# Kernel optimization log

Measured on AMD Instinct MI355X. Metric: run time of the kernel, lower is better.

The kernel has to match this reference:

```python
import jax, jax.numpy as jnp
import numpy as np

N_NODES = 50000
N_REL = 3
N_EDGES = 400000


def _graph_conv(x, src, dst, W, b, n_nodes):
    """DGL GraphConv with norm='both': D_out^-1/2 gather-sum D_in^-1/2 (x W) + b."""
    ones = jnp.ones(src.shape[0], dtype=x.dtype)
    deg_out = jnp.clip(jax.ops.segment_sum(ones, src, num_segments=n_nodes), 1.0)
    deg_in = jnp.clip(jax.ops.segment_sum(ones, dst, num_segments=n_nodes), 1.0)
    h = x * jax.lax.rsqrt(deg_out)[:, None]          # [N, F_in] src-side norm
    h = h @ W                                        # [N, F_out] project before aggregate
    m = jax.ops.segment_sum(h[src], dst, num_segments=n_nodes)  # SpMM message passing
    return m * jax.lax.rsqrt(deg_in)[:, None] + b


def setup_inputs() -> dict:
    key = jax.random.key(0)
    k = jax.random.split(key, 6)
    x = jax.random.normal(k[0], (N_NODES, 128), dtype=jnp.float32)
    edges = jax.random.randint(k[1], (N_REL, 2, N_EDGES), 0, N_NODES, dtype=jnp.int32)
    W1 = jax.random.normal(k[2], (N_REL, 128, 128), dtype=jnp.float32) * (1.0 / np.sqrt(128))
    b1 = jnp.zeros((N_REL, 128), dtype=jnp.float32)
    W2 = jax.random.normal(k[3], (N_REL, 128, 64), dtype=jnp.float32) * (1.0 / np.sqrt(128))
    b2 = jnp.zeros((N_REL, 64), dtype=jnp.float32)
    return {"x": x, "edges": edges, "W1": W1, "b1": b1, "W2": W2, "b2": b2}


def reference(x, edges, W1, b1, W2, b2):
    n = x.shape[0]
    # Layer 1: HeteroGraphConv(sum over relations) then ReLU
    h = jnp.zeros((n, W1.shape[-1]), dtype=x.dtype)
    for r in range(N_REL):
        h = h + _graph_conv(x, edges[r, 0], edges[r, 1], W1[r], b1[r], n)
    h = jax.nn.relu(h)
    # Layer 2 (conv6): HeteroGraphConv(sum over relations)
    out = jnp.zeros((n, W2.shape[-1]), dtype=x.dtype)
    for r in range(N_REL):
        out = out + _graph_conv(h, edges[r, 0], edges[r, 1], W2[r], b2[r], n)
    return out
```

## Files before the change

### kernel.cpp

```cpp
#include <hip/hip_runtime.h>

constexpr int NN = 50000;
constexpr int NREL = 3;
constexpr int NE = 400000;
constexpr int CAP = 24;
constexpr int MAXSPILL = 4096;

constexpr int G1X = (NN + 63) / 64;
constexpr int GEMM1_BLKS = G1X * 2 * NREL;
constexpr int LDA = 68;

__device__ __forceinline__ float b2f(unsigned short u) {
  union { unsigned int i; float f; } v; v.i = (unsigned int)u << 16; return v.f;
}
__device__ __forceinline__ unsigned short f2b(float f) {
  union { float f; unsigned int i; } v; v.f = f;
  unsigned int r = v.i + 0x7fffu + ((v.i >> 16) & 1u);
  return (unsigned short)(r >> 16);
}

template <bool SCALE, bool INBF>
__device__ __forceinline__ void gemm_body(
    const void* __restrict__ Av, const float* __restrict__ W,
    const int* __restrict__ cnt_scale, unsigned short* __restrict__ C,
    int M, int N, int row0, int col0) {
  __shared__ float As[64][LDA];
  __shared__ float Bs[64][64];
  int t = threadIdx.x;
  int tx4 = (t & 15) << 2;
  int ty4 = (t >> 4) << 2;
  float acc[4][4] = {};
  for (int k0 = 0; k0 < 128; k0 += 64) {
    if (k0) __syncthreads();
#pragma unroll
    for (int i = 0; i < 4; ++i) {
      int idx = t + i * 256;
      int r = idx >> 4;
      int c4 = (idx & 15) << 2;
      int grow = row0 + r;
      float4 v = make_float4(0.f, 0.f, 0.f, 0.f);
      if (grow < M) {
        if (INBF) {
          ushort4 u = *(const ushort4*)((const unsigned short*)Av + (size_t)grow * 128 + k0 + c4);
          v = make_float4(b2f(u.x), b2f(u.y), b2f(u.z), b2f(u.w));
        } else {
          v = *(const float4*)((const float*)Av + (size_t)grow * 128 + k0 + c4);
        }
        if (SCALE) {
          float s = rsqrtf((float)max(cnt_scale[grow], 1));
          v.x *= s; v.y *= s; v.z *= s; v.w *= s;
        }
      }
      *(float4*)(&As[r][c4]) = v;
    }
#pragma unroll
    for (int i = 0; i < 4; ++i) {
      int idx = t + i * 256;
      int k = idx >> 4;
      int c4 = (idx & 15) << 2;
      *(float4*)(&Bs[k][c4]) = *(const float4*)(W + (size_t)(k0 + k) * N + col0 + c4);
    }
    __syncthreads();
#pragma unroll 8
    for (int k = 0; k < 64; k += 4) {
      float4 b0 = *(const float4*)(&Bs[k + 0][tx4]);
      float4 b1 = *(const float4*)(&Bs[k + 1][tx4]);
      float4 b2 = *(const float4*)(&Bs[k + 2][tx4]);
      float4 b3 = *(const float4*)(&Bs[k + 3][tx4]);
#pragma unroll
      for (int m = 0; m < 4; ++m) {
        float4 a = *(const float4*)(&As[ty4 + m][k]);
        acc[m][0] += a.x * b0.x + a.y * b1.x + a.z * b2.x + a.w * b3.x;
        acc[m][1] += a.x * b0.y + a.y * b1.y + a.z * b2.y + a.w * b3.y;
        acc[m][2] += a.x * b0.z + a.y * b1.z + a.z * b2.z + a.w * b3.z;
        acc[m][3] += a.x * b0.w + a.y * b1.w + a.z * b2.w + a.w * b3.w;
      }
    }
  }
#pragma unroll
  for (int m = 0; m < 4; ++m) {
    int row = row0 + ty4 + m;
    if (row < M) {
      ushort4 o;
      o.x = f2b(acc[m][0]); o.y = f2b(acc[m][1]);
      o.z = f2b(acc[m][2]); o.w = f2b(acc[m][3]);
      *(ushort4*)(C + (size_t)row * N + col0 + tx4) = o;
    }
  }
}

__global__ __launch_bounds__(256, 3) void fused_build_gemm1_kernel(
    const int* __restrict__ edges, int* __restrict__ cnt_out, int* __restrict__ cnt_in,
    unsigned short* __restrict__ ell, int* __restrict__ nspill, int* __restrict__ spill,
    const float* __restrict__ x, const float* __restrict__ W1, unsigned short* __restrict__ proj1) {
  __shared__ float As[64][LDA];
  __shared__ float Bs[64][64];
  int t = threadIdx.x;

  int eg = blockIdx.x * 256 + t;
  bool have = (eg < NREL * NE);
  int er = 0, es = 0, ed = 0;
  if (have) {
    er = eg / NE;
    int e = eg - er * NE;
    const int* b = edges + (size_t)er * 2 * NE;
    es = b[e];
    ed = b[NE + e];
  }

  int g = blockIdx.x;
  int r = g / (G1X * 2);
  int rem = g - r * (G1X * 2);
  int row0 = (rem >> 1) * 64;
  int col0 = (rem & 1) * 64;
  const float* W = W1 + (size_t)r * 128 * 128;
  unsigned short* C = proj1 + (size_t)r * NN * 128;

  int tx4 = (t & 15) << 2;
  int ty4 = (t >> 4) << 2;
  float acc[4][4] = {};
  int pos = 0;
  for (int k0 = 0; k0 < 128; k0 += 64) {
    if (k0) __syncthreads();
#pragma unroll
    for (int i = 0; i < 4; ++i) {
      int idx = t + i * 256;
      int rr = idx >> 4;
      int c4 = (idx & 15) << 2;
      int grow = row0 + rr;
      float4 v = make_float4(0.f, 0.f, 0.f, 0.f);
      if (grow < NN) v = *(const float4*)(x + (size_t)grow * 128 + k0 + c4);
      *(float4*)(&As[rr][c4]) = v;
    }
#pragma unroll
    for (int i = 0; i < 4; ++i) {
      int idx = t + i * 256;
      int k = idx >> 4;
      int c4 = (idx & 15) << 2;
      *(float4*)(&Bs[k][c4]) = *(const float4*)(W + (size_t)(k0 + k) * 128 + col0 + c4);
    }
    __syncthreads();
    if (k0 == 0 && have) {
      atomicAdd(cnt_out + er * NN + es, 1);
      pos = atomicAdd(cnt_in + er * NN + ed, 1);
    }
#pragma unroll 8
    for (int k = 0; k < 64; k += 4) {
      float4 b0 = *(const float4*)(&Bs[k + 0][tx4]);
      float4 b1 = *(const float4*)(&Bs[k + 1][tx4]);
      float4 b2 = *(const float4*)(&Bs[k + 2][tx4]);
      float4 b3 = *(const float4*)(&Bs[k + 3][tx4]);
#pragma unroll
      for (int m = 0; m < 4; ++m) {
        float4 a = *(const float4*)(&As[ty4 + m][k]);
        acc[m][0] += a.x * b0.x + a.y * b1.x + a.z * b2.x + a.w * b3.x;
        acc[m][1] += a.x * b0.y + a.y * b1.y + a.z * b2.y + a.w * b3.y;
        acc[m][2] += a.x * b0.z + a.y * b1.z + a.z * b2.z + a.w * b3.z;
        acc[m][3] += a.x * b0.w + a.y * b1.w + a.z * b2.w + a.w * b3.w;
      }
    }
  }
#pragma unroll
  for (int m = 0; m < 4; ++m) {
    int row = row0 + ty4 + m;
    if (row < NN) {
      ushort4 o;
      o.x = f2b(acc[m][0]); o.y = f2b(acc[m][1]);
      o.z = f2b(acc[m][2]); o.w = f2b(acc[m][3]);
      *(ushort4*)(C + (size_t)row * 128 + col0 + tx4) = o;
    }
  }

  if (have) {
    if (pos < CAP) {
      ell[((size_t)er * NN + ed) * CAP + pos] = (unsigned short)es;
    } else {
      int i = atomicAdd(nspill, 1);
      if (i < MAXSPILL) { spill[3 * i] = er; spill[3 * i + 1] = ed; spill[3 * i + 2] = es; }
    }
  }
}

__global__ __launch_bounds__(256, 3) void gemm1_single_kernel(
    const float* __restrict__ x, const float* __restrict__ W1r, unsigned short* __restrict__ proj) {
  gemm_body<false, false>(x, W1r, nullptr, proj, NN, 128, blockIdx.x * 64, blockIdx.y * 64);
}
__global__ __launch_bounds__(256, 3) void gemm2_kernel(
    const unsigned short* __restrict__ h, const float* __restrict__ W2,
    const int* __restrict__ cnt_out, unsigned short* __restrict__ proj2, int relStride) {
  int r = blockIdx.z;
  gemm_body<true, true>(h, W2 + (size_t)r * 128 * 64, cnt_out + r * NN,
                        proj2 + (size_t)r * relStride, NN, 64, blockIdx.x * 64, 0);
}

__global__ void ell_build_kernel(const int* __restrict__ edges,
                                 int* __restrict__ cnt_out, int* __restrict__ cnt_in,
                                 unsigned short* __restrict__ ell,
                                 int* __restrict__ nspill, int* __restrict__ spill) {
  int gid = blockIdx.x * blockDim.x + threadIdx.x;
  if (gid >= NREL * NE) return;
  int r = gid / NE;
  int e = gid - r * NE;
  const int* b = edges + (size_t)r * 2 * NE;
  int s = b[e];
  int d = b[NE + e];
  atomicAdd(cnt_out + r * NN + s, 1);
  int pos = atomicAdd(cnt_in + r * NN + d, 1);
  if (pos < CAP) {
    ell[((size_t)r * NN + d) * CAP + pos] = (unsigned short)s;
  } else {
    int i = atomicAdd(nspill, 1);
    if (i < MAXSPILL) { spill[3 * i] = r; spill[3 * i + 1] = d; spill[3 * i + 2] = s; }
  }
}

__global__ __launch_bounds__(256) void agg1_all_kernel(
    const unsigned short* __restrict__ proj1, const unsigned short* __restrict__ ell,
    const int* __restrict__ cnt_in, const int* __restrict__ cnt_out,
    const int* __restrict__ nspill, const int* __restrict__ spill,
    const float* __restrict__ b1, unsigned short* __restrict__ h) {
  int row = (blockIdx.x * blockDim.x + threadIdx.x) >> 5;
  if (row >= NN) return;
  int lane = threadIdx.x & 31;
  int f = lane * 4;
  float4 q0 = *(const float4*)(b1 + f);
  float4 q1 = *(const float4*)(b1 + 128 + f);
  float4 q2 = *(const float4*)(b1 + 256 + f);
  float4 acc = make_float4(q0.x + q1.x + q2.x, q0.y + q1.y + q2.y,
                           q0.z + q1.z + q2.z, q0.w + q1.w + q2.w);
  int ns = min(*nspill, MAXSPILL);
  for (int r = 0; r < NREL; ++r) {
    const unsigned short* P = proj1 + (size_t)r * NN * 128;
    const int* co = cnt_out + r * NN;
    int deg = cnt_in[r * NN + row];
    int n = min(deg, CAP);
    const unsigned short* er = ell + ((size_t)r * NN + row) * CAP;
    float4 a0 = make_float4(0.f, 0.f, 0.f, 0.f);
    float4 a1 = make_float4(0.f, 0.f, 0.f, 0.f);
    int e = 0;
    for (; e + 1 < n; e += 2) {
      int s0 = er[e], s1 = er[e + 1];
      float w0 = rsqrtf((float)max(co[s0], 1));
      float w1 = rsqrtf((float)max(co[s1], 1));
      ushort4 u0 = *(const ushort4*)(P + (size_t)s0 * 128 + f);
      ushort4 u1 = *(const ushort4*)(P + (size_t)s1 * 128 + f);
      a0.x += w0 * b2f(u0.x); a0.y += w0 * b2f(u0.y); a0.z += w0 * b2f(u0.z); a0.w += w0 * b2f(u0.w);
      a1.x += w1 * b2f(u1.x); a1.y += w1 * b2f(u1.y); a1.z += w1 * b2f(u1.z); a1.w += w1 * b2f(u1.w);
    }
    if (e < n) {
      int s0 = er[e];
      float w0 = rsqrtf((float)max(co[s0], 1));
      ushort4 u0 = *(const ushort4*)(P + (size_t)s0 * 128 + f);
      a0.x += w0 * b2f(u0.x); a0.y += w0 * b2f(u0.y); a0.z += w0 * b2f(u0.z); a0.w += w0 * b2f(u0.w);
    }
    for (int i = 0; i < ns; ++i) {
      if (spill[3 * i] == r && spill[3 * i + 1] == row) {
        int s0 = spill[3 * i + 2];
        float w0 = rsqrtf((float)max(co[s0], 1));
        ushort4 u0 = *(const ushort4*)(P + (size_t)s0 * 128 + f);
        a0.x += w0 * b2f(u0.x); a0.y += w0 * b2f(u0.y); a0.z += w0 * b2f(u0.z); a0.w += w0 * b2f(u0.w);
      }
    }
    float si = rsqrtf((float)max(deg, 1));
    acc.x += (a0.x + a1.x) * si; acc.y += (a0.y + a1.y) * si;
    acc.z += (a0.z + a1.z) * si; acc.w += (a0.w + a1.w) * si;
  }
  ushort4 o;
  o.x = f2b(fmaxf(acc.x, 0.f)); o.y = f2b(fmaxf(acc.y, 0.f));
  o.z = f2b(fmaxf(acc.z, 0.f)); o.w = f2b(fmaxf(acc.w, 0.f));
  *(ushort4*)(h + (size_t)row * 128 + f) = o;
}

template <bool FIRST, bool LAST>
__global__ __launch_bounds__(256) void agg1_one_kernel(
    const unsigned short* __restrict__ P, const unsigned short* __restrict__ ell_r,
    const int* __restrict__ ci, const int* __restrict__ co,
    const int* __restrict__ nspill, const int* __restrict__ spill,
    int rel, const float* __restrict__ b1, unsigned short* __restrict__ h) {
  int row = (blockIdx.x * blockDim.x + threadIdx.x) >> 5;
  if (row >= NN) return;
  int lane = threadIdx.x & 31;
  int f = lane * 4;
  int deg = ci[row];
  int n = min(deg, CAP);
  const unsigned short* er = ell_r + (size_t)row * CAP;
  float4 a0 = make_float4(0.f, 0.f, 0.f, 0.f);
  for (int e = 0; e < n; ++e) {
    int s0 = er[e];
    float w0 = rsqrtf((float)max(co[s0], 1));
    ushort4 u0 = *(const ushort4*)(P + (size_t)s0 * 128 + f);
    a0.x += w0 * b2f(u0.x); a0.y += w0 * b2f(u0.y); a0.z += w0 * b2f(u0.z); a0.w += w0 * b2f(u0.w);
  }
  int ns = min(*nspill, MAXSPILL);
  for (int i = 0; i < ns; ++i) {
    if (spill[3 * i] == rel && spill[3 * i + 1] == row) {
      int s0 = spill[3 * i + 2];
      float w0 = rsqrtf((float)max(co[s0], 1));
      ushort4 u0 = *(const ushort4*)(P + (size_t)s0 * 128 + f);
      a0.x += w0 * b2f(u0.x); a0.y += w0 * b2f(u0.y); a0.z += w0 * b2f(u0.z); a0.w += w0 * b2f(u0.w);
    }
  }
  float si = rsqrtf((float)max(deg, 1));
  float4 acc;
  if (FIRST) {
    float4 q0 = *(const float4*)(b1 + f);
    float4 q1 = *(const float4*)(b1 + 128 + f);
    float4 q2 = *(const float4*)(b1 + 256 + f);
    acc = make_float4(q0.x + q1.x + q2.x, q0.y + q1.y + q2.y,
                      q0.z + q1.z + q2.z, q0.w + q1.w + q2.w);
  } else {
    ushort4 u = *(const ushort4*)(h + (size_t)row * 128 + f);
    acc = make_float4(b2f(u.x), b2f(u.y), b2f(u.z), b2f(u.w));
  }
  acc.x += a0.x * si; acc.y += a0.y * si; acc.z += a0.z * si; acc.w += a0.w * si;
  if (LAST) {
    acc.x = fmaxf(acc.x, 0.f); acc.y = fmaxf(acc.y, 0.f);
    acc.z = fmaxf(acc.z, 0.f); acc.w = fmaxf(acc.w, 0.f);
  }
  ushort4 o;
  o.x = f2b(acc.x); o.y = f2b(acc.y); o.z = f2b(acc.z); o.w = f2b(acc.w);
  *(ushort4*)(h + (size_t)row * 128 + f) = o;
}

__global__ __launch_bounds__(256) void agg2_all_kernel(
    const unsigned short* __restrict__ proj2, const unsigned short* __restrict__ ell,
    const int* __restrict__ cnt_in,
    const int* __restrict__ nspill, const int* __restrict__ spill,
    const float* __restrict__ b2, float* __restrict__ out) {
  int row = (blockIdx.x * blockDim.x + threadIdx.x) >> 4;
  if (row >= NN) return;
  int lane = threadIdx.x & 15;
  int f = lane * 4;
  float4 q0 = *(const float4*)(b2 + f);
  float4 q1 = *(const float4*)(b2 + 64 + f);
  float4 q2 = *(const float4*)(b2 + 128 + f);
  float4 acc = make_float4(q0.x + q1.x + q2.x, q0.y + q1.y + q2.y,
                           q0.z + q1.z + q2.z, q0.w + q1.w + q2.w);
  int ns = min(*nspill, MAXSPILL);
  for (int r = 0; r < NREL; ++r) {
    const unsigned short* P = proj2 + (size_t)r * NN * 64;
    int deg = cnt_in[r * NN + row];
    int n = min(deg, CAP);
    const unsigned short* er = ell + ((size_t)r * NN + row) * CAP;
    float4 a0 = make_float4(0.f, 0.f, 0.f, 0.f);
    float4 a1 = make_float4(0.f, 0.f, 0.f, 0.f);
    int e = 0;
    for (; e + 1 < n; e += 2) {
      int s0 = er[e], s1 = er[e + 1];
      ushort4 u0 = *(const ushort4*)(P + (size_t)s0 * 64 + f);
      ushort4 u1 = *(const ushort4*)(P + (size_t)s1 * 64 + f);
      a0.x += b2f(u0.x); a0.y += b2f(u0.y); a0.z += b2f(u0.z); a0.w += b2f(u0.w);
      a1.x += b2f(u1.x); a1.y += b2f(u1.y); a1.z += b2f(u1.z); a1.w += b2f(u1.w);
    }
    if (e < n) {
      int s0 = er[e];
      ushort4 u0 = *(const ushort4*)(P + (size_t)s0 * 64 + f);
      a0.x += b2f(u0.x); a0.y += b2f(u0.y); a0.z += b2f(u0.z); a0.w += b2f(u0.w);
    }
    for (int i = 0; i < ns; ++i) {
      if (spill[3 * i] == r && spill[3 * i + 1] == row) {
        int s0 = spill[3 * i + 2];
        ushort4 u0 = *(const ushort4*)(P + (size_t)s0 * 64 + f);
        a0.x += b2f(u0.x); a0.y += b2f(u0.y); a0.z += b2f(u0.z); a0.w += b2f(u0.w);
      }
    }
    float si = rsqrtf((float)max(deg, 1));
    acc.x += (a0.x + a1.x) * si; acc.y += (a0.y + a1.y) * si;
    acc.z += (a0.z + a1.z) * si; acc.w += (a0.w + a1.w) * si;
  }
  *(float4*)(out + (size_t)row * 64 + f) = acc;
}

template <bool FIRST>
__global__ __launch_bounds__(256) void agg2_one_kernel(
    const unsigned short* __restrict__ P, const unsigned short* __restrict__ ell_r,
    const int* __restrict__ ci,
    const int* __restrict__ nspill, const int* __restrict__ spill,
    int rel, const float* __restrict__ b2, float* __restrict__ out) {
  int row = (blockIdx.x * blockDim.x + threadIdx.x) >> 4;
  if (row >= NN) return;
  int lane = threadIdx.x & 15;
  int f = lane * 4;
  int deg = ci[row];
  int n = min(deg, CAP);
  const unsigned short* er = ell_r + (size_t)row * CAP;
  float4 a0 = make_float4(0.f, 0.f, 0.f, 0.f);
  for (int e = 0; e < n; ++e) {
    int s0 = er[e];
    ushort4 u0 = *(const ushort4*)(P + (size_t)s0 * 64 + f);
    a0.x += b2f(u0.x); a0.y += b2f(u0.y); a0.z += b2f(u0.z); a0.w += b2f(u0.w);
  }
  int ns = min(*nspill, MAXSPILL);
  for (int i = 0; i < ns; ++i) {
    if (spill[3 * i] == rel && spill[3 * i + 1] == row) {
      int s0 = spill[3 * i + 2];
      ushort4 u0 = *(const ushort4*)(P + (size_t)s0 * 64 + f);
      a0.x += b2f(u0.x); a0.y += b2f(u0.y); a0.z += b2f(u0.z); a0.w += b2f(u0.w);
    }
  }
  float si = rsqrtf((float)max(deg, 1));
  float4 acc;
  if (FIRST) {
    float4 q0 = *(const float4*)(b2 + f);
    float4 q1 = *(const float4*)(b2 + 64 + f);
    float4 q2 = *(const float4*)(b2 + 128 + f);
    acc = make_float4(q0.x + q1.x + q2.x, q0.y + q1.y + q2.y,
                      q0.z + q1.z + q2.z, q0.w + q1.w + q2.w);
  } else {
    acc = *(const float4*)(out + (size_t)row * 64 + f);
  }
  acc.x += a0.x * si; acc.y += a0.y * si; acc.z += a0.z * si; acc.w += a0.w * si;
  *(float4*)(out + (size_t)row * 64 + f) = acc;
}

extern "C" void kernel_launch(void* const* d_in, const int* in_sizes, int n_in,
                              void* d_out, int out_size, void* d_ws, size_t ws_size,
                              hipStream_t stream) {
  const float* x   = (const float*)d_in[0];
  const int* edges = (const int*)d_in[1];
  const float* W1  = (const float*)d_in[2];
  const float* b1  = (const float*)d_in[3];
  const float* W2  = (const float*)d_in[4];
  const float* b2  = (const float*)d_in[5];
  float* out = (float*)d_out;
  char* wsb = (char*)d_ws;

  const size_t PROJ_FULL = (size_t)NREL * NN * 128 * 2;
  const size_t PROJ_ONE  = (size_t)NN * 128 * 2;
  const size_t H_BYTES   = (size_t)NN * 128 * 2;
  const size_t ELL_BYTES = (size_t)NREL * NN * CAP * 2;
  const size_t CNT_BYTES = (size_t)NREL * NN * 4;
  const size_t FULL_NEED = PROJ_FULL + H_BYTES + ELL_BYTES + 2 * CNT_BYTES + 16 + 3 * MAXSPILL * 4;
  bool full = ws_size >= FULL_NEED;

  size_t projBytes = full ? PROJ_FULL : PROJ_ONE;
  unsigned short* proj = (unsigned short*)wsb;
  unsigned short* h    = (unsigned short*)(wsb + projBytes);
  unsigned short* ell  = (unsigned short*)(wsb + projBytes + H_BYTES);
  int* cnt_out = (int*)(wsb + projBytes + H_BYTES + ELL_BYTES);
  int* cnt_in  = cnt_out + NREL * NN;
  int* nspill  = cnt_in + NREL * NN;
  int* spill   = nspill + 4;

  hipMemsetAsync(cnt_out, 0, 2 * CNT_BYTES + 16, stream);

  const int agg1Blocks = (NN * 32 + 255) / 256;
  const int agg2Blocks = (NN * 16 + 255) / 256;

  if (full) {
    fused_build_gemm1_kernel<<<GEMM1_BLKS, 256, 0, stream>>>(
        edges, cnt_out, cnt_in, ell, nspill, spill, x, W1, proj);
    agg1_all_kernel<<<agg1Blocks, 256, 0, stream>>>(
        proj, ell, cnt_in, cnt_out, nspill, spill, b1, h);
    gemm2_kernel<<<dim3(G1X, 1, NREL), 256, 0, stream>>>(h, W2, cnt_out, proj, NN * 64);
    agg2_all_kernel<<<agg2Blocks, 256, 0, stream>>>(
        proj, ell, cnt_in, nspill, spill, b2, out);
  } else {
    ell_build_kernel<<<(NREL * NE + 255) / 256, 256, 0, stream>>>(
        edges, cnt_out, cnt_in, ell, nspill, spill);
    for (int r = 0; r < NREL; ++r) {
      gemm1_single_kernel<<<dim3(G1X, 2), 256, 0, stream>>>(
          x, W1 + (size_t)r * 128 * 128, proj);
      unsigned short* ell_r = ell + (size_t)r * NN * CAP;
      if (r == 0)
        agg1_one_kernel<true, false><<<agg1Blocks, 256, 0, stream>>>(
            proj, ell_r, cnt_in + r * NN, cnt_out + r * NN, nspill, spill, r, b1, h);
      else if (r == 1)
        agg1_one_kernel<false, false><<<agg1Blocks, 256, 0, stream>>>(
            proj, ell_r, cnt_in + r * NN, cnt_out + r * NN, nspill, spill, r, b1, h);
      else
        agg1_one_kernel<false, true><<<agg1Blocks, 256, 0, stream>>>(
            proj, ell_r, cnt_in + r * NN, cnt_out + r * NN, nspill, spill, r, b1, h);
    }
    for (int r = 0; r < NREL; ++r) {
      gemm2_kernel<<<dim3(G1X, 1, 1), 256, 0, stream>>>(
          h, W2 + (size_t)r * 128 * 64, cnt_out + r * NN, proj, 0);
      unsigned short* ell_r = ell + (size_t)r * NN * CAP;
      if (r == 0)
        agg2_one_kernel<true><<<agg2Blocks, 256, 0, stream>>>(
            proj, ell_r, cnt_in + r * NN, nspill, spill, r, b2, out);
      else
        agg2_one_kernel<false><<<agg2Blocks, 256, 0, stream>>>(
            proj, ell_r, cnt_in + r * NN, nspill, spill, r, b2, out);
    }
  }
}
```

Before: 268.9 us.

## Replicate degree counters and ELL lists per XCC with workgroup-scope atomics

Degree counters and ELL adjacency slots are replicated eight ways, indexed by the XCC id read from a hardware register. The build kernel then uses workgroup-scope relaxed atomics that only need to resolve in the local die's L2, instead of device-scope atomics. A new reduction kernel sums the replicated counts. The aggregation kernels walk all eight small per-replica lists. The old low-workspace multi-launch path and the 2-way unrolled gather loops are removed. In exchange it adds a much larger memset, an extra kernel launch, and more scattered ELL reads, and it depends on workgroup-scope atomics staying correct across workgroups on the same XCC.

```diff
diff --git a/kernel.cpp b/kernel.cpp
--- a/kernel.cpp
+++ b/kernel.cpp
@@ -3,12 +3,14 @@
 constexpr int NN = 50000;
 constexpr int NREL = 3;
 constexpr int NE = 400000;
-constexpr int CAP = 24;
 constexpr int MAXSPILL = 4096;
 
 constexpr int G1X = (NN + 63) / 64;
 constexpr int GEMM1_BLKS = G1X * 2 * NREL;
 constexpr int LDA = 68;
+constexpr int CAP8 = 10;
+constexpr int CAP1 = 24;
+constexpr size_t CS = (size_t)2 * NREL * NN;
 
 __device__ __forceinline__ float b2f(unsigned short u) {
   union { unsigned int i; float f; } v; v.i = (unsigned int)u << 16; return v.f;
@@ -89,13 +91,21 @@
   }
 }
 
+template <int R, int CAPR, bool WG>
 __global__ __launch_bounds__(256, 3) void fused_build_gemm1_kernel(
-    const int* __restrict__ edges, int* __restrict__ cnt_out, int* __restrict__ cnt_in,
-    unsigned short* __restrict__ ell, int* __restrict__ nspill, int* __restrict__ spill,
+    const int* __restrict__ edges, int* __restrict__ cnt8,
+    unsigned short* __restrict__ ell8, int* __restrict__ nspill, int* __restrict__ spill,
     const float* __restrict__ x, const float* __restrict__ W1, unsigned short* __restrict__ proj1) {
   __shared__ float As[64][LDA];
   __shared__ float Bs[64][64];
   int t = threadIdx.x;
+
+  int rep = 0;
+  if (R > 1) {
+    unsigned int xcc;
+    asm volatile("s_getreg_b32 %0, hwreg(HW_REG_XCC_ID)" : "=s"(xcc));
+    rep = (int)(xcc & (unsigned)(R - 1));
+  }
 
   int eg = blockIdx.x * 256 + t;
   bool have = (eg < NREL * NE);
@@ -141,8 +151,15 @@
     }
     __syncthreads();
     if (k0 == 0 && have) {
-      atomicAdd(cnt_out + er * NN + es, 1);
-      pos = atomicAdd(cnt_in + er * NN + ed, 1);
+      int* pout = cnt8 + rep * CS + (size_t)er * NN + es;
+      int* pin  = cnt8 + rep * CS + (size_t)NREL * NN + (size_t)er * NN + ed;
+      if (WG) {
+        __hip_atomic_fetch_add(pout, 1, __ATOMIC_RELAXED, __HIP_MEMORY_SCOPE_WORKGROUP);
+        pos = __hip_atomic_fetch_add(pin, 1, __ATOMIC_RELAXED, __HIP_MEMORY_SCOPE_WORKGROUP);
+      } else {
+        atomicAdd(pout, 1);
+        pos = atomicAdd(pin, 1);
+      }
     }
 #pragma unroll 8
     for (int k = 0; k < 64; k += 4) {
@@ -172,8 +189,8 @@
   }
 
   if (have) {
-    if (pos < CAP) {
-      ell[((size_t)er * NN + ed) * CAP + pos] = (unsigned short)es;
+    if (pos < CAPR) {
+      ell8[(((size_t)rep * NREL + er) * NN + ed) * CAPR + pos] = (unsigned short)es;
     } else {
       int i = atomicAdd(nspill, 1);
       if (i < MAXSPILL) { spill[3 * i] = er; spill[3 * i + 1] = ed; spill[3 * i + 2] = es; }
@@ -181,44 +198,27 @@
   }
 }
 
-__global__ __launch_bounds__(256, 3) void gemm1_single_kernel(
-    const float* __restrict__ x, const float* __restrict__ W1r, unsigned short* __restrict__ proj) {
-  gemm_body<false, false>(x, W1r, nullptr, proj, NN, 128, blockIdx.x * 64, blockIdx.y * 64);
-}
+__global__ void reduce_counts_kernel(const int* __restrict__ cnt8, int* __restrict__ cnt, int reps) {
+  int i = blockIdx.x * blockDim.x + threadIdx.x;
+  if (i >= (int)CS) return;
+  int s = 0;
+  for (int rr = 0; rr < reps; ++rr) s += cnt8[rr * CS + i];
+  cnt[i] = s;
+}
+
 __global__ __launch_bounds__(256, 3) void gemm2_kernel(
     const unsigned short* __restrict__ h, const float* __restrict__ W2,
-    const int* __restrict__ cnt_out, unsigned short* __restrict__ proj2, int relStride) {
+    const int* __restrict__ cnt, unsigned short* __restrict__ proj2) {
   int r = blockIdx.z;
-  gemm_body<true, true>(h, W2 + (size_t)r * 128 * 64, cnt_out + r * NN,
-                        proj2 + (size_t)r * relStride, NN, 64, blockIdx.x * 64, 0);
-}
-
-__global__ void ell_build_kernel(const int* __restrict__ edges,
-                                 int* __restrict__ cnt_out, int* __restrict__ cnt_in,
-                                 unsigned short* __restrict__ ell,
-                                 int* __restrict__ nspill, int* __restrict__ spill) {
-  int gid = blockIdx.x * blockDim.x + threadIdx.x;
-  if (gid >= NREL * NE) return;
-  int r = gid / NE;
-  int e = gid - r * NE;
-  const int* b = edges + (size_t)r * 2 * NE;
-  int s = b[e];
-  int d = b[NE + e];
-  atomicAdd(cnt_out + r * NN + s, 1);
-  int pos = atomicAdd(cnt_in + r * NN + d, 1);
-  if (pos < CAP) {
-    ell[((size_t)r * NN + d) * CAP + pos] = (unsigned short)s;
-  } else {
-    int i = atomicAdd(nspill, 1);
-    if (i < MAXSPILL) { spill[3 * i] = r; spill[3 * i + 1] = d; spill[3 * i + 2] = s; }
-  }
+  gemm_body<true, true>(h, W2 + (size_t)r * 128 * 64, cnt + (size_t)r * NN,
+                        proj2 + (size_t)r * NN * 64, NN, 64, blockIdx.x * 64, 0);
 }
 
 __global__ __launch_bounds__(256) void agg1_all_kernel(
-    const unsigned short* __restrict__ proj1, const unsigned short* __restrict__ ell,
-    const int* __restrict__ cnt_in, const int* __restrict__ cnt_out,
+    const unsigned short* __restrict__ proj1, const unsigned short* __restrict__ ell8,
+    const int* __restrict__ cnt8, const int* __restrict__ cnt,
     const int* __restrict__ nspill, const int* __restrict__ spill,
-    const float* __restrict__ b1, unsigned short* __restrict__ h) {
+    const float* __restrict__ b1, unsigned short* __restrict__ h, int reps, int capr) {
   int row = (blockIdx.x * blockDim.x + threadIdx.x) >> 5;
   if (row >= NN) return;
   int lane = threadIdx.x & 31;
@@ -231,39 +231,32 @@
   int ns = min(*nspill, MAXSPILL);
   for (int r = 0; r < NREL; ++r) {
     const unsigned short* P = proj1 + (size_t)r * NN * 128;
-    const int* co = cnt_out + r * NN;
-    int deg = cnt_in[r * NN + row];
-    int n = min(deg, CAP);
-    const unsigned short* er = ell + ((size_t)r * NN + row) * CAP;
+    const int* co = cnt + (size_t)r * NN;
+    int deg = cnt[NREL * NN + (size_t)r * NN + row];
     float4 a0 = make_float4(0.f, 0.f, 0.f, 0.f);
-    float4 a1 = make_float4(0.f, 0.f, 0.f, 0.f);
-    int e = 0;
-    for (; e + 1 < n; e += 2) {
-      int s0 = er[e], s1 = er[e + 1];
-      float w0 = rsqrtf((float)max(co[s0], 1));
-      float w1 = rsqrtf((float)max(co[s1], 1));
-      ushort4 u0 = *(const ushort4*)(P + (size_t)s0 * 128 + f);
-      ushort4 u1 = *(const ushort4*)(P + (size_t)s1 * 128 + f);
-      a0.x += w0 * b2f(u0.x); a0.y += w0 * b2f(u0.y); a0.z += w0 * b2f(u0.z); a0.w += w0 * b2f(u0.w);
-      a1.x += w1 * b2f(u1.x); a1.y += w1 * b2f(u1.y); a1.z += w1 * b2f(u1.z); a1.w += w1 * b2f(u1.w);
-    }
-    if (e < n) {
-      int s0 = er[e];
-      float w0 = rsqrtf((float)max(co[s0], 1));
-      ushort4 u0 = *(const ushort4*)(P + (size_t)s0 * 128 + f);
-      a0.x += w0 * b2f(u0.x); a0.y += w0 * b2f(u0.y); a0.z += w0 * b2f(u0.z); a0.w += w0 * b2f(u0.w);
+    for (int rep = 0; rep < reps; ++rep) {
+      int n = min(cnt8[rep * CS + NREL * NN + (size_t)r * NN + row], capr);
+      const unsigned short* er = ell8 + (((size_t)rep * NREL + r) * NN + row) * capr;
+      for (int e = 0; e < n; ++e) {
+        int s0 = er[e];
+        float w0 = rsqrtf((float)max(co[s0], 1));
+        ushort4 u0 = *(const ushort4*)(P + (size_t)s0 * 128 + f);
+        a0.x += w0 * b2f(u0.x); a0.y += w0 * b2f(u0.y);
+        a0.z += w0 * b2f(u0.z); a0.w += w0 * b2f(u0.w);
+      }
     }
     for (int i = 0; i < ns; ++i) {
       if (spill[3 * i] == r && spill[3 * i + 1] == row) {
         int s0 = spill[3 * i + 2];
         float w0 = rsqrtf((float)max(co[s0], 1));
         ushort4 u0 = *(const ushort4*)(P + (size_t)s0 * 128 + f);
-        a0.x += w0 * b2f(u0.x); a0.y += w0 * b2f(u0.y); a0.z += w0 * b2f(u0.z); a0.w += w0 * b2f(u0.w);
+        a0.x += w0 * b2f(u0.x); a0.y += w0 * b2f(u0.y);
+        a0.z += w0 * b2f(u0.z); a0.w += w0 * b2f(u0.w);
       }
     }
     float si = rsqrtf((float)max(deg, 1));
-    acc.x += (a0.x + a1.x) * si; acc.y += (a0.y + a1.y) * si;
-    acc.z += (a0.z + a1.z) * si; acc.w += (a0.w + a1.w) * si;
+    acc.x += a0.x * si; acc.y += a0.y * si;
+    acc.z += a0.z * si; acc.w += a0.w * si;
   }
   ushort4 o;
   o.x = f2b(fmaxf(acc.x, 0.f)); o.y = f2b(fmaxf(acc.y, 0.f));
@@ -271,62 +264,11 @@
   *(ushort4*)(h + (size_t)row * 128 + f) = o;
 }
 
-template <bool FIRST, bool LAST>
-__global__ __launch_bounds__(256) void agg1_one_kernel(
-    const unsigned short* __restrict__ P, const unsigned short* __restrict__ ell_r,
-    const int* __restrict__ ci, const int* __restrict__ co,
+__global__ __launch_bounds__(256) void agg2_all_kernel(
+    const unsigned short* __restrict__ proj2, const unsigned short* __restrict__ ell8,
+    const int* __restrict__ cnt8, const int* __restrict__ cnt,
     const int* __restrict__ nspill, const int* __restrict__ spill,
-    int rel, const float* __restrict__ b1, unsigned short* __restrict__ h) {
-  int row = (blockIdx.x * blockDim.x + threadIdx.x) >> 5;
-  if (row >= NN) return;
-  int lane = threadIdx.x & 31;
-  int f = lane * 4;
-  int deg = ci[row];
-  int n = min(deg, CAP);
-  const unsigned short* er = ell_r + (size_t)row * CAP;
-  float4 a0 = make_float4(0.f, 0.f, 0.f, 0.f);
-  for (int e = 0; e < n; ++e) {
-    int s0 = er[e];
-    float w0 = rsqrtf((float)max(co[s0], 1));
-    ushort4 u0 = *(const ushort4*)(P + (size_t)s0 * 128 + f);
-    a0.x += w0 * b2f(u0.x); a0.y += w0 * b2f(u0.y); a0.z += w0 * b2f(u0.z); a0.w += w0 * b2f(u0.w);
-  }
-  int ns = min(*nspill, MAXSPILL);
-  for (int i = 0; i < ns; ++i) {
-    if (spill[3 * i] == rel && spill[3 * i + 1] == row) {
-      int s0 = spill[3 * i + 2];
-      float w0 = rsqrtf((float)max(co[s0], 1));
-      ushort4 u0 = *(const ushort4*)(P + (size_t)s0 * 128 + f);
-      a0.x += w0 * b2f(u0.x); a0.y += w0 * b2f(u0.y); a0.z += w0 * b2f(u0.z); a0.w += w0 * b2f(u0.w);
-    }
-  }
-  float si = rsqrtf((float)max(deg, 1));
-  float4 acc;
-  if (FIRST) {
-    float4 q0 = *(const float4*)(b1 + f);
-    float4 q1 = *(const float4*)(b1 + 128 + f);
-    float4 q2 = *(const float4*)(b1 + 256 + f);
-    acc = make_float4(q0.x + q1.x + q2.x, q0.y + q1.y + q2.y,
-                      q0.z + q1.z + q2.z, q0.w + q1.w + q2.w);
-  } else {
-    ushort4 u = *(const ushort4*)(h + (size_t)row * 128 + f);
-    acc = make_float4(b2f(u.x), b2f(u.y), b2f(u.z), b2f(u.w));
-  }
-  acc.x += a0.x * si; acc.y += a0.y * si; acc.z += a0.z * si; acc.w += a0.w * si;
-  if (LAST) {
-    acc.x = fmaxf(acc.x, 0.f); acc.y = fmaxf(acc.y, 0.f);
-    acc.z = fmaxf(acc.z, 0.f); acc.w = fmaxf(acc.w, 0.f);
-  }
-  ushort4 o;
-  o.x = f2b(acc.x); o.y = f2b(acc.y); o.z = f2b(acc.z); o.w = f2b(acc.w);
-  *(ushort4*)(h + (size_t)row * 128 + f) = o;
-}
-
-__global__ __launch_bounds__(256) void agg2_all_kernel(
-    const unsigned short* __restrict__ proj2, const unsigned short* __restrict__ ell,
-    const int* __restrict__ cnt_in,
-    const int* __restrict__ nspill, const int* __restrict__ spill,
-    const float* __restrict__ b2, float* __restrict__ out) {
+    const float* __restrict__ b2, float* __restrict__ out, int reps, int capr) {
   int row = (blockIdx.x * blockDim.x + threadIdx.x) >> 4;
   if (row >= NN) return;
   int lane = threadIdx.x & 15;
@@ -339,23 +281,16 @@
   int ns = min(*nspill, MAXSPILL);
   for (int r = 0; r < NREL; ++r) {
     const unsigned short* P = proj2 + (size_t)r * NN * 64;
-    int deg = cnt_in[r * NN + row];
-    int n = min(deg, CAP);
-    const unsigned short* er = ell + ((size_t)r * NN + row) * CAP;
+    int deg = cnt[NREL * NN + (size_t)r * NN + row];
     float4 a0 = make_float4(0.f, 0.f, 0.f, 0.f);
-    float4 a1 = make_float4(0.f, 0.f, 0.f, 0.f);
-    int e = 0;
-    for (; e + 1 < n; e += 2) {
-      int s0 = er[e], s1 = er[e + 1];
-      ushort4 u0 = *(const ushort4*)(P + (size_t)s0 * 64 + f);
-      ushort4 u1 = *(const ushort4*)(P + (size_t)s1 * 64 + f);
-      a0.x += b2f(u0.x); a0.y += b2f(u0.y); a0.z += b2f(u0.z); a0.w += b2f(u0.w);
-      a1.x += b2f(u1.x); a1.y += b2f(u1.y); a1.z += b2f(u1.z); a1.w += b2f(u1.w);
-    }
-    if (e < n) {
-      int s0 = er[e];
-      ushort4 u0 = *(const ushort4*)(P + (size_t)s0 * 64 + f);
-      a0.x += b2f(u0.x); a0.y += b2f(u0.y); a0.z += b2f(u0.z); a0.w += b2f(u0.w);
+    for (int rep = 0; rep < reps; ++rep) {
+      int n = min(cnt8[rep * CS + NREL * NN + (size_t)r * NN + row], capr);
+      const unsigned short* er = ell8 + (((size_t)rep * NREL + r) * NN + row) * capr;
+      for (int e = 0; e < n; ++e) {
+        int s0 = er[e];
+        ushort4 u0 = *(const ushort4*)(P + (size_t)s0 * 64 + f);
+        a0.x += b2f(u0.x); a0.y += b2f(u0.y); a0.z += b2f(u0.z); a0.w += b2f(u0.w);
+      }
     }
     for (int i = 0; i < ns; ++i) {
       if (spill[3 * i] == r && spill[3 * i + 1] == row) {
@@ -365,51 +300,9 @@
       }
     }
     float si = rsqrtf((float)max(deg, 1));
-    acc.x += (a0.x + a1.x) * si; acc.y += (a0.y + a1.y) * si;
-    acc.z += (a0.z + a1.z) * si; acc.w += (a0.w + a1.w) * si;
-  }
-  *(float4*)(out + (size_t)row * 64 + f) = acc;
-}
-
-template <bool FIRST>
-__global__ __launch_bounds__(256) void agg2_one_kernel(
-    const unsigned short* __restrict__ P, const unsigned short* __restrict__ ell_r,
-    const int* __restrict__ ci,
-    const int* __restrict__ nspill, const int* __restrict__ spill,
-    int rel, const float* __restrict__ b2, float* __restrict__ out) {
-  int row = (blockIdx.x * blockDim.x + threadIdx.x) >> 4;
-  if (row >= NN) return;
-  int lane = threadIdx.x & 15;
-  int f = lane * 4;
-  int deg = ci[row];
-  int n = min(deg, CAP);
-  const unsigned short* er = ell_r + (size_t)row * CAP;
-  float4 a0 = make_float4(0.f, 0.f, 0.f, 0.f);
-  for (int e = 0; e < n; ++e) {
-    int s0 = er[e];
-    ushort4 u0 = *(const ushort4*)(P + (size_t)s0 * 64 + f);
-    a0.x += b2f(u0.x); a0.y += b2f(u0.y); a0.z += b2f(u0.z); a0.w += b2f(u0.w);
-  }
-  int ns = min(*nspill, MAXSPILL);
-  for (int i = 0; i < ns; ++i) {
-    if (spill[3 * i] == rel && spill[3 * i + 1] == row) {
-      int s0 = spill[3 * i + 2];
-      ushort4 u0 = *(const ushort4*)(P + (size_t)s0 * 64 + f);
-      a0.x += b2f(u0.x); a0.y += b2f(u0.y); a0.z += b2f(u0.z); a0.w += b2f(u0.w);
-    }
-  }
-  float si = rsqrtf((float)max(deg, 1));
-  float4 acc;
-  if (FIRST) {
-    float4 q0 = *(const float4*)(b2 + f);
-    float4 q1 = *(const float4*)(b2 + 64 + f);
-    float4 q2 = *(const float4*)(b2 + 128 + f);
-    acc = make_float4(q0.x + q1.x + q2.x, q0.y + q1.y + q2.y,
-                      q0.z + q1.z + q2.z, q0.w + q1.w + q2.w);
-  } else {
-    acc = *(const float4*)(out + (size_t)row * 64 + f);
-  }
-  acc.x += a0.x * si; acc.y += a0.y * si; acc.z += a0.z * si; acc.w += a0.w * si;
+    acc.x += a0.x * si; acc.y += a0.y * si;
+    acc.z += a0.z * si; acc.w += a0.w * si;
+  }
   *(float4*)(out + (size_t)row * 64 + f) = acc;
 }
 
@@ -425,63 +318,40 @@
   float* out = (float*)d_out;
   char* wsb = (char*)d_ws;
 
-  const size_t PROJ_FULL = (size_t)NREL * NN * 128 * 2;
-  const size_t PROJ_ONE  = (size_t)NN * 128 * 2;
-  const size_t H_BYTES   = (size_t)NN * 128 * 2;
-  const size_t ELL_BYTES = (size_t)NREL * NN * CAP * 2;
-  const size_t CNT_BYTES = (size_t)NREL * NN * 4;
-  const size_t FULL_NEED = PROJ_FULL + H_BYTES + ELL_BYTES + 2 * CNT_BYTES + 16 + 3 * MAXSPILL * 4;
-  bool full = ws_size >= FULL_NEED;
-
-  size_t projBytes = full ? PROJ_FULL : PROJ_ONE;
+  const size_t PROJ_B = (size_t)NREL * NN * 128 * 2;
+  const size_t H_B    = (size_t)NN * 128 * 2;
+  auto need = [&](int R, int CAPR) {
+    return PROJ_B + H_B + (size_t)R * NREL * NN * CAPR * 2 +
+           (size_t)R * CS * 4 + 16 + (size_t)3 * MAXSPILL * 4 + CS * 4;
+  };
+  int R = (ws_size >= need(8, CAP8)) ? 8 : 1;
+  int CAPR = (R == 8) ? CAP8 : CAP1;
+
   unsigned short* proj = (unsigned short*)wsb;
-  unsigned short* h    = (unsigned short*)(wsb + projBytes);
-  unsigned short* ell  = (unsigned short*)(wsb + projBytes + H_BYTES);
-  int* cnt_out = (int*)(wsb + projBytes + H_BYTES + ELL_BYTES);
-  int* cnt_in  = cnt_out + NREL * NN;
-  int* nspill  = cnt_in + NREL * NN;
-  int* spill   = nspill + 4;
-
-  hipMemsetAsync(cnt_out, 0, 2 * CNT_BYTES + 16, stream);
+  unsigned short* h    = (unsigned short*)(wsb + PROJ_B);
+  unsigned short* ell8 = (unsigned short*)(wsb + PROJ_B + H_B);
+  size_t ellB = (size_t)R * NREL * NN * CAPR * 2;
+  int* cnt8   = (int*)(wsb + PROJ_B + H_B + ellB);
+  int* nspill = cnt8 + (size_t)R * CS;
+  int* spill  = nspill + 4;
+  int* cnt    = spill + 3 * MAXSPILL;
+
+  hipMemsetAsync(cnt8, 0, (size_t)R * CS * 4 + 16, stream);
 
   const int agg1Blocks = (NN * 32 + 255) / 256;
   const int agg2Blocks = (NN * 16 + 255) / 256;
 
-  if (full) {
-    fused_build_gemm1_kernel<<<GEMM1_BLKS, 256, 0, stream>>>(
-        edges, cnt_out, cnt_in, ell, nspill, spill, x, W1, proj);
-    agg1_all_kernel<<<agg1Blocks, 256, 0, stream>>>(
-        proj, ell, cnt_in, cnt_out, nspill, spill, b1, h);
-    gemm2_kernel<<<dim3(G1X, 1, NREL), 256, 0, stream>>>(h, W2, cnt_out, proj, NN * 64);
-    agg2_all_kernel<<<agg2Blocks, 256, 0, stream>>>(
-        proj, ell, cnt_in, nspill, spill, b2, out);
+  if (R == 8) {
+    fused_build_gemm1_kernel<8, CAP8, true><<<GEMM1_BLKS, 256, 0, stream>>>(
+        edges, cnt8, ell8, nspill, spill, x, W1, proj);
   } else {
-    ell_build_kernel<<<(NREL * NE + 255) / 256, 256, 0, stream>>>(
-        edges, cnt_out, cnt_in, ell, nspill, spill);
-    for (int r = 0; r < NREL; ++r) {
-      gemm1_single_kernel<<<dim3(G1X, 2), 256, 0, stream>>>(
-          x, W1 + (size_t)r * 128 * 128, proj);
-      unsigned short* ell_r = ell + (size_t)r * NN * CAP;
-      if (r == 0)
-        agg1_one_kernel<true, false><<<agg1Blocks, 256, 0, stream>>>(
-            proj, ell_r, cnt_in + r * NN, cnt_out + r * NN, nspill, spill, r, b1, h);
-      else if (r == 1)
-        agg1_one_kernel<false, false><<<agg1Blocks, 256, 0, stream>>>(
-            proj, ell_r, cnt_in + r * NN, cnt_out + r * NN, nspill, spill, r, b1, h);
-      else
-        agg1_one_kernel<false, true><<<agg1Blocks, 256, 0, stream>>>(
-            proj, ell_r, cnt_in + r * NN, cnt_out + r * NN, nspill, spill, r, b1, h);
-    }
-    for (int r = 0; r < NREL; ++r) {
-      gemm2_kernel<<<dim3(G1X, 1, 1), 256, 0, stream>>>(
-          h, W2 + (size_t)r * 128 * 64, cnt_out + r * NN, proj, 0);
-      unsigned short* ell_r = ell + (size_t)r * NN * CAP;
-      if (r == 0)
-        agg2_one_kernel<true><<<agg2Blocks, 256, 0, stream>>>(
-            proj, ell_r, cnt_in + r * NN, nspill, spill, r, b2, out);
-      else
-        agg2_one_kernel<false><<<agg2Blocks, 256, 0, stream>>>(
-            proj, ell_r, cnt_in + r * NN, nspill, spill, r, b2, out);
-    }
-  }
-}
+    fused_build_gemm1_kernel<1, CAP1, false><<<GEMM1_BLKS, 256, 0, stream>>>(
+        edges, cnt8, ell8, nspill, spill, x, W1, proj);
+  }
+  reduce_counts_kernel<<<((int)CS + 255) / 256, 256, 0, stream>>>(cnt8, cnt, R);
+  agg1_all_kernel<<<agg1Blocks, 256, 0, stream>>>(
+      proj, ell8, cnt8, cnt, nspill, spill, b1, h, R, CAPR);
+  gemm2_kernel<<<dim3(G1X, 1, NREL), 256, 0, stream>>>(h, W2, cnt, proj);
+  agg2_all_kernel<<<agg2Blocks, 256, 0, stream>>>(
+      proj, ell8, cnt8, cnt, nspill, spill, b2, out, R, CAPR);
+}
```

Result: slower. 392.5 us (+46.0%).
